# Performance work log

Hardware: AMD Instinct MI355X
Metric: run time of the kernel (lower is better)

The kernel has to match this reference:

```python
import jax, jax.numpy as jnp
import numpy as np

NEG = -9e15

def setup_inputs() -> dict:
    key = jax.random.key(0)
    kH, kA, kW, ka = jax.random.split(key, 4)
    B, N, Din, Dout, Hh = 4, 2048, 128, 32, 8
    H = jax.random.normal(kH, (B, N, Din), dtype=jnp.float32)
    adj = jax.random.randint(kA, (B, N, N), 0, 2, dtype=jnp.int32)
    W = jax.random.normal(kW, (Hh, Din, Dout), dtype=jnp.float32) * (1.0 / np.sqrt(Din))
    a = jax.random.normal(ka, (Hh, 2 * Dout, 1), dtype=jnp.float32) * 0.1
    return {"H": H, "adj": adj, "W": W, "a": a}

def reference(H, adj, W, a):
    # H: [B,N,Din], adj: [B,N,N], W: [h,Din,D], a: [h,2D,1]
    B, N, _ = H.shape
    h, _, D = W.shape
    Wh = jnp.einsum('bni,hio->bhno', H, W)            # [B,h,N,D]
    a1 = a[:, :D, 0]                                   # [h,D] (source/query half)
    a2 = a[:, D:, 0]                                   # [h,D] (neighbor half)
    ei = jnp.einsum('bhnd,hd->bhn', Wh, a1)            # [B,h,N]
    ej = jnp.einsum('bhnd,hd->bhn', Wh, a2)            # [B,h,N]
    e = ei[:, :, :, None] + ej[:, :, None, :]          # [B,h,N,N] == a^T[Wh_i;Wh_j]
    mask = adj[:, None, :, :].astype(bool)             # [B,1,N,N]
    e = jnp.where(mask, e, jnp.float32(NEG))
    alpha = jax.nn.softmax(e, axis=-1)                 # [B,h,N,N]; dropout is identity (eval)
    h_prime = jnp.einsum('bhnm,bhmd->bhnd', alpha, Wh) # [B,h,N,D]
    h_prime = jnp.transpose(h_prime, (0, 2, 1, 3)).reshape(B, N, h * D)
    return jax.nn.relu(h_prime), alpha
```

## Files before the change

### kernel.cpp

```cpp
#include <hip/hip_runtime.h>
#include <stdint.h>

#define BB 4
#define NN 2048
#define DIN 128
#define DOUT 32
#define HH 8
#define NW 64

typedef __bf16 bf16x8 __attribute__((ext_vector_type(8)));
typedef float  f32x4  __attribute__((ext_vector_type(4)));

static __device__ __forceinline__ unsigned short f2b(float f) {
    __bf16 h = (__bf16)f;
    return __builtin_bit_cast(unsigned short, h);
}

__global__ __launch_bounds__(256) void k_wht(const float* __restrict__ Hg,
                                             const float* __restrict__ Wg,
                                             const float* __restrict__ ag,
                                             unsigned short* __restrict__ WhT,
                                             float* __restrict__ E)
{
    __shared__ float Hs[DIN * 16];
    __shared__ float ejred[HH][16][36];
    const int t  = threadIdx.x;
    const int b  = blockIdx.x >> 7;
    const int n0 = (blockIdx.x & 127) << 4;

    {
        const int r = t >> 4, i0 = (t & 15) << 3;
        const float4* hp = (const float4*)(Hg + ((size_t)(b * NN + n0 + r)) * DIN + i0);
        float4 u0 = hp[0], u1 = hp[1];
        float vv[8] = { u0.x, u0.y, u0.z, u0.w, u1.x, u1.y, u1.z, u1.w };
#pragma unroll
        for (int j = 0; j < 8; j++) Hs[(i0 + j) * 16 + r] = vv[j];
    }
    __syncthreads();

    const int h = t >> 5, d = t & 31;
    f32x4 a0 = {0,0,0,0}, a1 = {0,0,0,0}, a2 = {0,0,0,0}, a3 = {0,0,0,0};
    const float* wp = Wg + h * DIN * DOUT + d;
#pragma unroll 8
    for (int i = 0; i < DIN; i++) {
        float wv = wp[i * DOUT];
        const f32x4* hr = (const f32x4*)&Hs[i * 16];
        a0 += wv * hr[0];
        a1 += wv * hr[1];
        a2 += wv * hr[2];
        a3 += wv * hr[3];
    }
    float v[16] = { a0[0],a0[1],a0[2],a0[3], a1[0],a1[1],a1[2],a1[3],
                    a2[0],a2[1],a2[2],a2[3], a3[0],a3[1],a3[2],a3[3] };
    unsigned int pw[8];
#pragma unroll
    for (int j = 0; j < 8; j++)
        pw[j] = (unsigned int)f2b(v[2*j]) | ((unsigned int)f2b(v[2*j+1]) << 16);
    uint4* dst = (uint4*)(WhT + ((size_t)((b * HH + h) * DOUT + d)) * NN + n0);
    dst[0] = make_uint4(pw[0], pw[1], pw[2], pw[3]);
    dst[1] = make_uint4(pw[4], pw[5], pw[6], pw[7]);

    const float a2v = ag[h * 2 * DOUT + DOUT + d];
#pragma unroll
    for (int j = 0; j < 16; j++) ejred[h][j][d] = v[j] * a2v;
    __syncthreads();
    if (t < 128) {
        const int hh = t >> 4, j = t & 15;
        const f32x4* rp = (const f32x4*)&ejred[hh][j][0];
        f32x4 s4 = rp[0] + rp[1] + rp[2] + rp[3] + rp[4] + rp[5] + rp[6] + rp[7];
        float s = s4[0] + s4[1] + s4[2] + s4[3];
        E[((size_t)(b * HH + hh)) * NN + n0 + j] = __expf(s);
    }
}

__global__ __launch_bounds__(256) void k_bits(const int* __restrict__ adj,
                                              unsigned long long* __restrict__ BM)
{
    size_t tg = (size_t)blockIdx.x * 256 + threadIdx.x;
    unsigned long long m = __ballot(adj[tg] != 0);
    if ((threadIdx.x & 63) == 0) BM[tg >> 6] = m;
}

__global__ __launch_bounds__(256) void k_main(const float* __restrict__ E,
                                              const unsigned int* __restrict__ BM,
                                              const unsigned short* __restrict__ WhT,
                                              float* __restrict__ out0,
                                              float* __restrict__ out1)
{
    __shared__ float        Es[NN];
    __shared__ unsigned int bits[16][68];
    __shared__ float        red[16][17];
    __shared__ float        invS[16];
    __shared__ float        Cred[4][16][33];

    const int t   = threadIdx.x;
    const int xcd = blockIdx.x & 7;
    const int j   = blockIdx.x >> 3;
    const int bh  = (xcd << 2) + (j >> 7);
    const int b   = bh >> 3, h = bh & 7;
    const int n0  = (j & 127) << 4;

    {
        const f32x4* src = (const f32x4*)(E + (size_t)bh * NN);
        f32x4* dst = (f32x4*)Es;
        dst[t]       = src[t];
        dst[t + 256] = src[t + 256];
        const int r = t >> 4, w0 = (t & 15) << 2;
        *(uint4*)&bits[r][w0] =
            *(const uint4*)(BM + ((size_t)(b * NN + n0 + r)) * NW + w0);
    }
    __syncthreads();

    {
        const int r = t >> 4, l = t & 15;
        const unsigned int* br = bits[r];
        float s = 0.f;
#pragma unroll 4
        for (int k2 = 0; k2 < NW; k2++) {
            unsigned int wd = br[k2];
            int m = (k2 << 5) + l;
            float v0 = Es[m], v1 = Es[m + 16];
            s += ((wd >> l) & 1)        ? v0 : 0.f;
            s += ((wd >> (l + 16)) & 1) ? v1 : 0.f;
        }
        red[r][l] = s;
    }
    __syncthreads();
    if (t < 16) {
        float s = 0.f;
#pragma unroll
        for (int jj = 0; jj < 16; jj++) s += red[t][jj];
        invS[t] = 1.0f / s;
    }
    __syncthreads();

    const int w = t >> 6, lane = t & 63;
    const int quad = lane >> 4, l16 = lane & 15;
    f32x4 acc[2] = { {0,0,0,0}, {0,0,0,0} };
    const float iv = invS[l16];
    float* o1 = out1 + ((size_t)bh * NN + n0 + l16) * NN;
    const unsigned short* wB0 = WhT + ((size_t)(bh * DOUT) + l16) * NN;
    const unsigned short* wB1 = wB0 + (size_t)16 * NN;

#pragma unroll 2
    for (int c = 0; c < 8; c++) {
        const int m0 = (w << 9) + (c << 6);
        const uint2 bw = *(const uint2*)&bits[l16][m0 >> 5];
        const unsigned int b0 = bw.x >> (quad << 3);
        const unsigned int b1 = bw.y >> (quad << 3);

        const int mA = m0 + (quad << 3);
        f32x4 e0 = *(const f32x4*)&Es[mA];
        f32x4 e1 = *(const f32x4*)&Es[mA + 4];
        f32x4 e2 = *(const f32x4*)&Es[mA + 32];
        f32x4 e3 = *(const f32x4*)&Es[mA + 36];
        f32x4 x0, x1, x2, x3;
#pragma unroll
        for (int jj = 0; jj < 4; jj++) {
            x0[jj] = ((b0 >> jj) & 1)       ? e0[jj] * iv : 0.f;
            x1[jj] = ((b0 >> (jj + 4)) & 1) ? e1[jj] * iv : 0.f;
            x2[jj] = ((b1 >> jj) & 1)       ? e2[jj] * iv : 0.f;
            x3[jj] = ((b1 >> (jj + 4)) & 1) ? e3[jj] * iv : 0.f;
        }
        *(f32x4*)(o1 + mA)      = x0;
        *(f32x4*)(o1 + mA + 4)  = x1;
        *(f32x4*)(o1 + mA + 32) = x2;
        *(f32x4*)(o1 + mA + 36) = x3;

        unsigned int pk[8] = {
            (unsigned int)f2b(x0[0]) | ((unsigned int)f2b(x0[1]) << 16),
            (unsigned int)f2b(x0[2]) | ((unsigned int)f2b(x0[3]) << 16),
            (unsigned int)f2b(x1[0]) | ((unsigned int)f2b(x1[1]) << 16),
            (unsigned int)f2b(x1[2]) | ((unsigned int)f2b(x1[3]) << 16),
            (unsigned int)f2b(x2[0]) | ((unsigned int)f2b(x2[1]) << 16),
            (unsigned int)f2b(x2[2]) | ((unsigned int)f2b(x2[3]) << 16),
            (unsigned int)f2b(x3[0]) | ((unsigned int)f2b(x3[1]) << 16),
            (unsigned int)f2b(x3[2]) | ((unsigned int)f2b(x3[3]) << 16) };
        bf16x8 af0 = __builtin_bit_cast(bf16x8, make_uint4(pk[0], pk[1], pk[2], pk[3]));
        bf16x8 af1 = __builtin_bit_cast(bf16x8, make_uint4(pk[4], pk[5], pk[6], pk[7]));

        bf16x8 b00 = __builtin_bit_cast(bf16x8, *(const uint4*)(wB0 + mA));
        bf16x8 b01 = __builtin_bit_cast(bf16x8, *(const uint4*)(wB0 + mA + 32));
        bf16x8 b10 = __builtin_bit_cast(bf16x8, *(const uint4*)(wB1 + mA));
        bf16x8 b11 = __builtin_bit_cast(bf16x8, *(const uint4*)(wB1 + mA + 32));

        acc[0] = __builtin_amdgcn_mfma_f32_16x16x32_bf16(af0, b00, acc[0], 0, 0, 0);
        acc[1] = __builtin_amdgcn_mfma_f32_16x16x32_bf16(af0, b10, acc[1], 0, 0, 0);
        acc[0] = __builtin_amdgcn_mfma_f32_16x16x32_bf16(af1, b01, acc[0], 0, 0, 0);
        acc[1] = __builtin_amdgcn_mfma_f32_16x16x32_bf16(af1, b11, acc[1], 0, 0, 0);
    }

#pragma unroll
    for (int hf = 0; hf < 2; hf++)
#pragma unroll
        for (int i = 0; i < 4; i++)
            Cred[w][(quad << 2) + i][l16 + (hf << 4)] = acc[hf][i];
    __syncthreads();
#pragma unroll
    for (int e = t; e < 512; e += 256) {
        const int r = e >> 5, d = e & 31;
        float v = Cred[0][r][d] + Cred[1][r][d] + Cred[2][r][d] + Cred[3][r][d];
        out0[((size_t)(b * NN + n0 + r)) * (HH * DOUT) + h * DOUT + d] = fmaxf(v, 0.f);
    }
}

extern "C" void kernel_launch(void* const* d_in, const int* in_sizes, int n_in,
                              void* d_out, int out_size, void* d_ws, size_t ws_size,
                              hipStream_t stream)
{
    const float* Hg  = (const float*)d_in[0];
    const int*   adj = (const int*)d_in[1];
    const float* Wg  = (const float*)d_in[2];
    const float* ag  = (const float*)d_in[3];

    float* out0 = (float*)d_out;
    float* out1 = out0 + (size_t)BB * NN * HH * DOUT;

    char* ws = (char*)d_ws;
    unsigned short* WhT = (unsigned short*)ws;
    float*          E   = (float*)(ws + (size_t)BB*HH*DOUT*NN*2);
    unsigned int*   BM  = (unsigned int*)(ws + (size_t)BB*HH*DOUT*NN*2
                                             + (size_t)BB*HH*NN*4);

    k_wht <<<BB * (NN/16),         256, 0, stream>>>(Hg, Wg, ag, WhT, E);
    k_bits<<<(BB * NN * NN) / 256, 256, 0, stream>>>(adj, (unsigned long long*)BM);
    k_main<<<BB * HH * (NN/16),    256, 0, stream>>>(E, BM, WhT, out0, out1);
}
```

Before: 647.5 us.

## Prefetch WhT operands, shuffle-reduce row sums, and alias shared memory in k_main

The first WhT B-operand tile is issued at kernel entry, before the E and bitmask loads, and inside the fully unrolled loop the next iteration's tile is loaded while the current one computes. The row-sum reduction now uses width-16 shuffles instead of a shared-memory pass, which removes one barrier. Shared memory is packed into one aliased buffer so the reduction area reuses the Es region, and the out1 stores move after the MFMAs. This is meant to hide global load latency and cut LDS use and barriers. In exchange it needs more registers and adds an extra barrier before the Cred writes.

```diff
diff --git a/kernel.cpp b/kernel.cpp
--- a/kernel.cpp
+++ b/kernel.cpp
@@ -87,18 +87,29 @@
                                               float* __restrict__ out0,
                                               float* __restrict__ out1)
 {
-    __shared__ float        Es[NN];
-    __shared__ unsigned int bits[16][68];
-    __shared__ float        red[16][17];
-    __shared__ float        invS[16];
-    __shared__ float        Cred[4][16][33];
+    __shared__ __align__(16) char smem[12608];
+    float*        Es   = (float*)smem;
+    unsigned int (*bits)[68] = (unsigned int (*)[68])(smem + 8192);
+    float*        invS = (float*)(smem + 8192 + 4352);
+    float (*Cred)[16][33] = (float (*)[16][33])smem;
 
     const int t   = threadIdx.x;
     const int xcd = blockIdx.x & 7;
-    const int j   = blockIdx.x >> 3;
-    const int bh  = (xcd << 2) + (j >> 7);
+    const int jx  = blockIdx.x >> 3;
+    const int bh  = (xcd << 2) + (jx >> 7);
     const int b   = bh >> 3, h = bh & 7;
-    const int n0  = (j & 127) << 4;
+    const int n0  = (jx & 127) << 4;
+
+    const int w = t >> 6, lane = t & 63;
+    const int quad = lane >> 4, l16 = lane & 15;
+
+    const unsigned short* wB0 = WhT + ((size_t)(bh * DOUT) + l16) * NN;
+    const unsigned short* wB1 = wB0 + (size_t)16 * NN;
+    const int mA0 = (w << 9) + (quad << 3);
+    uint4 B00 = *(const uint4*)(wB0 + mA0);
+    uint4 B01 = *(const uint4*)(wB0 + mA0 + 32);
+    uint4 B10 = *(const uint4*)(wB1 + mA0);
+    uint4 B11 = *(const uint4*)(wB1 + mA0 + 32);
 
     {
         const f32x4* src = (const f32x4*)(E + (size_t)bh * NN);
@@ -123,33 +134,35 @@
             s += ((wd >> l) & 1)        ? v0 : 0.f;
             s += ((wd >> (l + 16)) & 1) ? v1 : 0.f;
         }
-        red[r][l] = s;
-    }
-    __syncthreads();
-    if (t < 16) {
-        float s = 0.f;
-#pragma unroll
-        for (int jj = 0; jj < 16; jj++) s += red[t][jj];
-        invS[t] = 1.0f / s;
-    }
-    __syncthreads();
-
-    const int w = t >> 6, lane = t & 63;
-    const int quad = lane >> 4, l16 = lane & 15;
-    f32x4 acc[2] = { {0,0,0,0}, {0,0,0,0} };
+        s += __shfl_xor(s, 1, 16);
+        s += __shfl_xor(s, 2, 16);
+        s += __shfl_xor(s, 4, 16);
+        s += __shfl_xor(s, 8, 16);
+        if (l == 0) invS[r] = 1.0f / s;
+    }
+    __syncthreads();
+
+    f32x4 acc0 = {0,0,0,0}, acc1 = {0,0,0,0};
     const float iv = invS[l16];
     float* o1 = out1 + ((size_t)bh * NN + n0 + l16) * NN;
-    const unsigned short* wB0 = WhT + ((size_t)(bh * DOUT) + l16) * NN;
-    const unsigned short* wB1 = wB0 + (size_t)16 * NN;
-
-#pragma unroll 2
+
+#pragma unroll
     for (int c = 0; c < 8; c++) {
         const int m0 = (w << 9) + (c << 6);
+        const int mA = m0 + (quad << 3);
+
+        uint4 N00, N01, N10, N11;
+        if (c < 7) {
+            N00 = *(const uint4*)(wB0 + mA + 64);
+            N01 = *(const uint4*)(wB0 + mA + 96);
+            N10 = *(const uint4*)(wB1 + mA + 64);
+            N11 = *(const uint4*)(wB1 + mA + 96);
+        }
+
         const uint2 bw = *(const uint2*)&bits[l16][m0 >> 5];
         const unsigned int b0 = bw.x >> (quad << 3);
         const unsigned int b1 = bw.y >> (quad << 3);
 
-        const int mA = m0 + (quad << 3);
         f32x4 e0 = *(const f32x4*)&Es[mA];
         f32x4 e1 = *(const f32x4*)&Es[mA + 4];
         f32x4 e2 = *(const f32x4*)&Es[mA + 32];
@@ -162,10 +175,6 @@
             x2[jj] = ((b1 >> jj) & 1)       ? e2[jj] * iv : 0.f;
             x3[jj] = ((b1 >> (jj + 4)) & 1) ? e3[jj] * iv : 0.f;
         }
-        *(f32x4*)(o1 + mA)      = x0;
-        *(f32x4*)(o1 + mA + 4)  = x1;
-        *(f32x4*)(o1 + mA + 32) = x2;
-        *(f32x4*)(o1 + mA + 36) = x3;
 
         unsigned int pk[8] = {
             (unsigned int)f2b(x0[0]) | ((unsigned int)f2b(x0[1]) << 16),
@@ -179,22 +188,25 @@
         bf16x8 af0 = __builtin_bit_cast(bf16x8, make_uint4(pk[0], pk[1], pk[2], pk[3]));
         bf16x8 af1 = __builtin_bit_cast(bf16x8, make_uint4(pk[4], pk[5], pk[6], pk[7]));
 
-        bf16x8 b00 = __builtin_bit_cast(bf16x8, *(const uint4*)(wB0 + mA));
-        bf16x8 b01 = __builtin_bit_cast(bf16x8, *(const uint4*)(wB0 + mA + 32));
-        bf16x8 b10 = __builtin_bit_cast(bf16x8, *(const uint4*)(wB1 + mA));
-        bf16x8 b11 = __builtin_bit_cast(bf16x8, *(const uint4*)(wB1 + mA + 32));
-
-        acc[0] = __builtin_amdgcn_mfma_f32_16x16x32_bf16(af0, b00, acc[0], 0, 0, 0);
-        acc[1] = __builtin_amdgcn_mfma_f32_16x16x32_bf16(af0, b10, acc[1], 0, 0, 0);
-        acc[0] = __builtin_amdgcn_mfma_f32_16x16x32_bf16(af1, b01, acc[0], 0, 0, 0);
-        acc[1] = __builtin_amdgcn_mfma_f32_16x16x32_bf16(af1, b11, acc[1], 0, 0, 0);
-    }
-
-#pragma unroll
-    for (int hf = 0; hf < 2; hf++)
-#pragma unroll
-        for (int i = 0; i < 4; i++)
-            Cred[w][(quad << 2) + i][l16 + (hf << 4)] = acc[hf][i];
+        acc0 = __builtin_amdgcn_mfma_f32_16x16x32_bf16(af0, __builtin_bit_cast(bf16x8, B00), acc0, 0, 0, 0);
+        acc1 = __builtin_amdgcn_mfma_f32_16x16x32_bf16(af0, __builtin_bit_cast(bf16x8, B10), acc1, 0, 0, 0);
+        acc0 = __builtin_amdgcn_mfma_f32_16x16x32_bf16(af1, __builtin_bit_cast(bf16x8, B01), acc0, 0, 0, 0);
+        acc1 = __builtin_amdgcn_mfma_f32_16x16x32_bf16(af1, __builtin_bit_cast(bf16x8, B11), acc1, 0, 0, 0);
+
+        *(f32x4*)(o1 + mA)      = x0;
+        *(f32x4*)(o1 + mA + 4)  = x1;
+        *(f32x4*)(o1 + mA + 32) = x2;
+        *(f32x4*)(o1 + mA + 36) = x3;
+
+        if (c < 7) { B00 = N00; B01 = N01; B10 = N10; B11 = N11; }
+    }
+
+    __syncthreads();
+#pragma unroll
+    for (int i = 0; i < 4; i++) {
+        Cred[w][(quad << 2) + i][l16]      = acc0[i];
+        Cred[w][(quad << 2) + i][l16 + 16] = acc1[i];
+    }
     __syncthreads();
 #pragma unroll
     for (int e = t; e < 512; e += 256) {
```

Measured after the change: 642.3 us. About the same (-0.8%).
